# Kernel tuning notes

Measured on AMD Instinct MI355X. Metric: run time of the kernel, lower is better.

Reference implementation:

```python
import jax, jax.numpy as jnp
import numpy as np

N_IN, N_REC, T, BATCH = 128, 512, 1000, 64
ALPHA = 0.2
SIGMA = float(np.sqrt(2.0 / ALPHA) * 0.05)  # sqrt(2/alpha)*sigma_rec
EI_RATIO = 0.8
W_REC_GAIN = 1.0


def setup_inputs() -> dict:
    key = jax.random.key(0)
    k_x, k_n = jax.random.split(key)
    rng = np.random.RandomState(0)
    # w_in init: randn/sqrt(n_in)
    w_in = (rng.randn(N_IN, N_REC) / np.sqrt(N_IN)).astype(np.float32)
    # w_rec init 'randgauss' with Dale's law: abs, inhibitory rows scaled
    n_ex = int(N_REC * EI_RATIO)
    w_rec0 = W_REC_GAIN * rng.randn(N_REC, N_REC) / np.sqrt(N_REC)
    w_rec0 = np.abs(w_rec0)
    w_rec0[n_ex:, :] *= EI_RATIO / (1.0 - EI_RATIO)
    w_rec = w_rec0.astype(np.float32)
    ei_vec = np.concatenate([np.ones(n_ex), -np.ones(N_REC - n_ex)]).astype(np.float32)
    ei_mask = np.diag(ei_vec)
    autapse_mask = np.ones((N_REC, N_REC), dtype=np.float32)
    np.fill_diagonal(autapse_mask, 0.0)
    x = jax.random.normal(k_x, (BATCH, T, N_IN), dtype=jnp.float32)
    # pre-scaled noise: randn * sigma, one draw per timestep (matches torch.randn_like(h)*sigma)
    noise = jax.random.normal(k_n, (BATCH, T, N_REC), dtype=jnp.float32) * SIGMA
    return {
        "x": x,
        "w_in": jnp.asarray(w_in),
        "w_rec": jnp.asarray(w_rec),
        "b_rec": jnp.zeros((N_REC,), dtype=jnp.float32),
        "ei_mask": jnp.asarray(ei_mask),
        "autapse_mask": jnp.asarray(autapse_mask),
        "noise": noise,
    }


def reference(x, w_in, w_rec, b_rec, ei_mask, autapse_mask, noise):
    # Effective recurrent weight, computed ONCE (torch code recomputes each step)
    w_eff = ei_mask @ (w_rec * autapse_mask)          # (n_rec, n_rec)
    inp_all = jnp.einsum("bti,ir->btr", x, w_in)       # precompute input projection
    xs = (jnp.swapaxes(inp_all, 0, 1), jnp.swapaxes(noise, 0, 1))  # (T,b,r)
    h0 = jnp.zeros((x.shape[0], w_rec.shape[0]), dtype=x.dtype)

    def step(h, xt):
        inp_t, noise_t = xt
        pre = inp_t + h @ w_eff + b_rec + noise_t
        h_new = (1.0 - ALPHA) * h + ALPHA * jax.nn.relu(pre)
        return h_new, h_new

    _, h_all = jax.lax.scan(step, h0, xs)              # (T, batch, n_rec)
    return jnp.swapaxes(h_all, 0, 1)                   # (batch, T, n_rec)
```

## Files before the change

### kernel.cpp

```cpp
#include <hip/hip_runtime.h>

#define T_STEPS 1000
#define NIN     128
#define NREC    512
#define NBATCH  64
#define ALPHA   0.2f

#define NSLICE  4
#define SCOLS   128
#define NGRP    8
#define KPER    64

#define WS_W_OFF      0
#define WS_COMM_OFF   (1u << 20)
#define COMM_U64      (NBATCH * NREC)
#define COMM_BYTES    (2 * COMM_U64 * 8)
#define WS_COMM2_OFF  (WS_COMM_OFF + COMM_BYTES)
#define WS_NEEDED_LLC (WS_COMM_OFF + COMM_BYTES)
#define WS_NEEDED_DUAL (WS_COMM2_OFF + COMM_BYTES)

#define LDS_BARRIER() do {                                        \
    asm volatile("s_waitcnt lgkmcnt(0)" ::: "memory");            \
    __builtin_amdgcn_s_barrier();                                 \
    asm volatile("" ::: "memory");                                \
} while (0)

__device__ __forceinline__ unsigned long long ld_l2(
        const unsigned long long* p) {
    unsigned long long r;
    asm volatile("global_load_dwordx2 %0, %1, off sc0\n\t"
                 "s_waitcnt vmcnt(0)"
                 : "=v"(r) : "v"(p) : "memory");
    return r;
}
__device__ __forceinline__ void st_l2(unsigned long long* p,
                                      unsigned long long v) {
    asm volatile("global_store_dwordx2 %0, %1, off"
                 :: "v"(p), "v"(v) : "memory");
}
__device__ __forceinline__ unsigned long long ld_llc(
        const unsigned long long* p) {
    return __hip_atomic_load(p, __ATOMIC_RELAXED, __HIP_MEMORY_SCOPE_AGENT);
}
__device__ __forceinline__ void st_llc(unsigned long long* p,
                                       unsigned long long v) {
    __hip_atomic_store(p, v, __ATOMIC_RELAXED, __HIP_MEMORY_SCOPE_AGENT);
}

__global__ void weff_kernel(const float* __restrict__ w_rec,
                            const float* __restrict__ ei_mask,
                            const float* __restrict__ autapse,
                            float* __restrict__ w_eff) {
    int idx = blockIdx.x * blockDim.x + threadIdx.x;
    if (idx < NREC * NREC) {
        int row = idx >> 9;
        float ei = ei_mask[row * NREC + row];
        w_eff[idx] = ei * w_rec[idx] * autapse[idx];
    }
}

__global__ __launch_bounds__(1024) void gemm_in_kernel(
        const float* __restrict__ x,
        const float* __restrict__ w_in,
        const float* __restrict__ b_rec,
        float* __restrict__ io) {
    __shared__ float xs[32][NIN];

    const int tid = threadIdx.x;
    const int m0  = blockIdx.x * 32;

    {
        const float4* src = reinterpret_cast<const float4*>(x + (size_t)m0 * NIN);
        reinterpret_cast<float4*>(&xs[0][0])[tid] = src[tid];
    }
    __syncthreads();

    const int j0 = tid & 255;
    const int j1 = j0 + 256;
    const int rg = tid >> 8;

    float acc[8][2];
#pragma unroll
    for (int i = 0; i < 8; ++i) { acc[i][0] = 0.f; acc[i][1] = 0.f; }

#pragma unroll 4
    for (int k = 0; k < NIN; ++k) {
        float wv0 = w_in[k * NREC + j0];
        float wv1 = w_in[k * NREC + j1];
#pragma unroll
        for (int i = 0; i < 8; ++i) {
            float xv = xs[rg * 8 + i][k];
            acc[i][0] = fmaf(xv, wv0, acc[i][0]);
            acc[i][1] = fmaf(xv, wv1, acc[i][1]);
        }
    }

    const float br0 = b_rec[j0];
    const float br1 = b_rec[j1];
#pragma unroll
    for (int i = 0; i < 8; ++i) {
        size_t ro = (size_t)(m0 + rg * 8 + i) * NREC;
        io[ro + j0] = acc[i][0] + br0;
        io[ro + j1] = acc[i][1] + br1;
    }
}

__global__ __launch_bounds__(1024, 4) void rnn_coop(
        const float* __restrict__ W,
        const float* __restrict__ noise,
        float* __restrict__ io,
        unsigned long long* __restrict__ comm,
        unsigned long long* __restrict__ comm2) {
    __shared__ __align__(16) float h_lds[NREC];
    __shared__ float part[NGRP * SCOLS];

    const int tid = threadIdx.x;
    const int bid = blockIdx.x;
    const int b   = (bid & 7) + 8 * (bid >> 5);
    const int s   = (bid >> 3) & 3;
    const int jl  = tid & (SCOLS - 1);
    const int g   = tid >> 7;
    const int ln  = tid & 63;
    const int jg  = s * SCOLS + jl;
    const bool remote = (g >> 1) != s;
    const int cslot = g * KPER + ln;
    const bool use_l2 = (comm2 != nullptr);

    float Wr[KPER];
    {
        const float* wp = W + (size_t)(g * KPER) * NREC + jg;
#pragma unroll
        for (int u = 0; u < KPER; ++u)
            Wr[u] = wp[(size_t)u * NREC];
    }
#pragma unroll
    for (int u = 0; u < KPER; ++u)
        asm volatile("" : "+v"(Wr[u]));

    if (tid < NREC) h_lds[tid] = 0.f;
    __syncthreads();

    float hj = 0.f;
    const size_t iobase = (size_t)b * T_STEPS * NREC + jg;
    const unsigned long long* cbase  = comm  + (size_t)b * NREC + cslot;
    const unsigned long long* cbase2 = comm2 + (size_t)b * NREC + cslot;
    unsigned long long* cwr  = comm  + (size_t)b * NREC + jg;
    unsigned long long* cwr2 = comm2 + (size_t)b * NREC + jg;

    float inp = 0.f, nz = 0.f;
    if (tid < SCOLS) { inp = io[iobase]; nz = noise[iobase]; }

    for (int t = 0; t < T_STEPS; ++t) {
        const size_t off = iobase + (size_t)t * NREC;

        float inp_n = 0.f, nz_n = 0.f;
        if (t + 1 < T_STEPS && tid < SCOLS) {
            inp_n = io[off + NREC];
            nz_n  = noise[off + NREC];
        }

        if (t > 0 && remote) {
            const size_t po = (size_t)(t & 1) * COMM_U64;
            unsigned long long v;
            if (use_l2) {
                v = ld_l2(cbase2 + po);
                while ((int)(unsigned)(v >> 32) < t) {
                    v = ld_llc(cbase + po);
                    if ((int)(unsigned)(v >> 32) >= t) break;
                    v = ld_l2(cbase2 + po);
                }
            } else {
                v = ld_llc(cbase + po);
                while ((int)(unsigned)(v >> 32) < t)
                    v = ld_llc(cbase + po);
            }
            asm volatile("" ::: "memory");
            h_lds[cslot] = __uint_as_float((unsigned)(v & 0xffffffffu));
        }

        float a0 = 0.f, a1 = 0.f, a2 = 0.f, a3 = 0.f;
        const float4* h4 = reinterpret_cast<const float4*>(&h_lds[g * KPER]);
#pragma unroll
        for (int u = 0; u < KPER / 4; ++u) {
            float4 hv = h4[u];
            a0 = fmaf(hv.x, Wr[4 * u + 0], a0);
            a1 = fmaf(hv.y, Wr[4 * u + 1], a1);
            a2 = fmaf(hv.z, Wr[4 * u + 2], a2);
            a3 = fmaf(hv.w, Wr[4 * u + 3], a3);
        }
        part[g * SCOLS + jl] = (a0 + a1) + (a2 + a3);
        LDS_BARRIER();

        if (tid < SCOLS) {
            float pre = inp + nz;
#pragma unroll
            for (int q = 0; q < NGRP; ++q)
                pre += part[q * SCOLS + jl];
            float hnew = (1.f - ALPHA) * hj + ALPHA * fmaxf(pre, 0.f);
            hj = hnew;
            h_lds[jg] = hnew;
            unsigned long long pv =
                ((unsigned long long)(unsigned)(t + 1) << 32) |
                (unsigned long long)__float_as_uint(hnew);
            const size_t po = (size_t)((t + 1) & 1) * COMM_U64;
            if (use_l2) st_l2(cwr2 + po, pv);
            st_llc(cwr + po, pv);
            io[off] = hnew;
        }
        inp = inp_n; nz = nz_n;
        LDS_BARRIER();
    }
}

__global__ __launch_bounds__(1024) void rnn_kernel(
        const float* __restrict__ W,
        const float* __restrict__ noise,
        float* __restrict__ io) {
    __shared__ float h[NREC];
    __shared__ float part2[NREC];

    const int tid  = threadIdx.x;
    const int j    = tid & (NREC - 1);
    const int half = tid >> 9;
    const int b    = blockIdx.x;

    if (tid < NREC) h[tid] = 0.f;
    float hj = 0.f;
    __syncthreads();

    const int kb = half * 256;
    const float* wp = W + (size_t)kb * NREC + j;
    const size_t base = (size_t)b * T_STEPS * NREC + j;

    for (int t = 0; t < T_STEPS; ++t) {
        const size_t off = base + (size_t)t * NREC;
        float acc = (half == 0) ? (io[off] + noise[off]) : 0.f;
#pragma unroll
        for (int ku = 0; ku < 256; ku += 16) {
            float w[16];
#pragma unroll
            for (int u = 0; u < 16; ++u) w[u] = wp[(size_t)(ku + u) * NREC];
#pragma unroll
            for (int u = 0; u < 16; ++u) acc = fmaf(h[kb + ku + u], w[u], acc);
        }
        if (half == 1) part2[j] = acc;
        __syncthreads();
        if (half == 0) {
            float pre  = acc + part2[j];
            float hnew = (1.f - ALPHA) * hj + ALPHA * fmaxf(pre, 0.f);
            io[off] = hnew;
            h[j] = hnew;
            hj = hnew;
        }
        __syncthreads();
    }
}

extern "C" void kernel_launch(void* const* d_in, const int* in_sizes, int n_in,
                              void* d_out, int out_size, void* d_ws, size_t ws_size,
                              hipStream_t stream) {
    const float* x       = (const float*)d_in[0];
    const float* w_in    = (const float*)d_in[1];
    const float* w_rec   = (const float*)d_in[2];
    const float* b_rec   = (const float*)d_in[3];
    const float* ei_mask = (const float*)d_in[4];
    const float* autapse = (const float*)d_in[5];
    const float* noise   = (const float*)d_in[6];
    float* out = (float*)d_out;

    char* ws = (char*)d_ws;
    float* W = (float*)(ws + WS_W_OFF);
    unsigned long long* comm  = (unsigned long long*)(ws + WS_COMM_OFF);
    unsigned long long* comm2 = (unsigned long long*)(ws + WS_COMM2_OFF);

    weff_kernel<<<dim3((NREC * NREC + 255) / 256), dim3(256), 0, stream>>>(
        w_rec, ei_mask, autapse, W);

    gemm_in_kernel<<<dim3(64000 / 32), dim3(1024), 0, stream>>>(
        x, w_in, b_rec, out);

    if (ws_size >= (size_t)WS_NEEDED_DUAL) {
        hipMemsetAsync(comm, 0, 2 * COMM_BYTES, stream);
        void* args[] = {(void*)&W, (void*)&noise, (void*)&out,
                        (void*)&comm, (void*)&comm2};
        hipLaunchCooperativeKernel(reinterpret_cast<void*>(rnn_coop),
                                   dim3(NBATCH * NSLICE), dim3(1024),
                                   args, 0, stream);
    } else if (ws_size >= (size_t)WS_NEEDED_LLC) {
        hipMemsetAsync(comm, 0, COMM_BYTES, stream);
        unsigned long long* nul = nullptr;
        void* args[] = {(void*)&W, (void*)&noise, (void*)&out,
                        (void*)&comm, (void*)&nul};
        hipLaunchCooperativeKernel(reinterpret_cast<void*>(rnn_coop),
                                   dim3(NBATCH * NSLICE), dim3(1024),
                                   args, 0, stream);
    } else {
        rnn_kernel<<<dim3(NBATCH), dim3(1024), 0, stream>>>(W, noise, out);
    }
}
```

Baseline: 1.754 ms.

## Offload next-step input/noise prefetch to non-remote waves via LDS double buffer

Moves the per-step prefetch of the next timestep's input projection and noise from the 128 finalizing threads to the 256 local (non-remote) threads, staged through a double-buffered LDS array. The finalizing wave no longer carries global-load latency on the critical path. It also changes the spin-wait polling to hit the L2 copy three times for every LLC probe. The risk is extra LDS traffic, and polling the LLC less often could delay noticing a new value when the L2 copy is stale.

```diff
diff --git a/kernel.cpp b/kernel.cpp
--- a/kernel.cpp
+++ b/kernel.cpp
@@ -113,6 +113,7 @@
         unsigned long long* __restrict__ comm2) {
     __shared__ __align__(16) float h_lds[NREC];
     __shared__ float part[NGRP * SCOLS];
+    __shared__ float ldsin[2][2][SCOLS];
 
     const int tid = threadIdx.x;
     const int bid = blockIdx.x;
@@ -126,6 +127,13 @@
     const int cslot = g * KPER + ln;
     const bool use_l2 = (comm2 != nullptr);
 
+    const int  lt        = tid - s * 256;
+    const bool is_loader = (lt >= 0) && (lt < 256);
+    const int  lwhich    = (lt >> 7) & 1;
+    const int  lcol      = lt & (SCOLS - 1);
+    const float* lsrc    = lwhich ? noise : io;
+    const size_t lbase   = (size_t)b * T_STEPS * NREC + s * SCOLS + lcol;
+
     float Wr[KPER];
     {
         const float* wp = W + (size_t)(g * KPER) * NREC + jg;
@@ -138,6 +146,7 @@
         asm volatile("" : "+v"(Wr[u]));
 
     if (tid < NREC) h_lds[tid] = 0.f;
+    if (is_loader) ldsin[0][lwhich][lcol] = lsrc[lbase];
     __syncthreads();
 
     float hj = 0.f;
@@ -147,27 +156,26 @@
     unsigned long long* cwr  = comm  + (size_t)b * NREC + jg;
     unsigned long long* cwr2 = comm2 + (size_t)b * NREC + jg;
 
-    float inp = 0.f, nz = 0.f;
-    if (tid < SCOLS) { inp = io[iobase]; nz = noise[iobase]; }
-
     for (int t = 0; t < T_STEPS; ++t) {
-        const size_t off = iobase + (size_t)t * NREC;
-
-        float inp_n = 0.f, nz_n = 0.f;
-        if (t + 1 < T_STEPS && tid < SCOLS) {
-            inp_n = io[off + NREC];
-            nz_n  = noise[off + NREC];
-        }
+        const int p = t & 1;
+
+        float lv = 0.f;
+        const bool lactive = is_loader && (t + 1 < T_STEPS);
+        if (lactive)
+            lv = lsrc[lbase + (size_t)(t + 1) * NREC];
 
         if (t > 0 && remote) {
-            const size_t po = (size_t)(t & 1) * COMM_U64;
+            const size_t po = (size_t)p * COMM_U64;
             unsigned long long v;
             if (use_l2) {
                 v = ld_l2(cbase2 + po);
+                int it = 0;
                 while ((int)(unsigned)(v >> 32) < t) {
-                    v = ld_llc(cbase + po);
-                    if ((int)(unsigned)(v >> 32) >= t) break;
-                    v = ld_l2(cbase2 + po);
+                    if ((++it & 3) == 0) {
+                        v = ld_llc(cbase + po);
+                    } else {
+                        v = ld_l2(cbase2 + po);
+                    }
                 }
             } else {
                 v = ld_llc(cbase + po);
@@ -192,6 +200,8 @@
         LDS_BARRIER();
 
         if (tid < SCOLS) {
+            float inp = ldsin[p][0][jl];
+            float nz  = ldsin[p][1][jl];
             float pre = inp + nz;
 #pragma unroll
             for (int q = 0; q < NGRP; ++q)
@@ -205,9 +215,12 @@
             const size_t po = (size_t)((t + 1) & 1) * COMM_U64;
             if (use_l2) st_l2(cwr2 + po, pv);
             st_llc(cwr + po, pv);
-            io[off] = hnew;
-        }
-        inp = inp_n; nz = nz_n;
+            io[iobase + (size_t)t * NREC] = hnew;
+        }
+
+        if (lactive)
+            ldsin[p ^ 1][lwhich][lcol] = lv;
+
         LDS_BARRIER();
     }
 }
```

Result: slower. 2.330 ms (+32.9%).

## Broadcast hidden state via wave readlane instead of LDS staging in coop RNN

Applied to the files above, without the earlier changes.

Each wave now loads its 64 hidden values into one register per lane, either by polling the remote comm buffer or from a small own-slice LDS array. It then broadcasts them with readlane into the FMA loop, replacing the full 512-float LDS h buffer and the float4 LDS reads. The thread-to-column mapping changes so each wave covers 64 columns of one K-group. The next step's input and noise prefetch moves to after the store, inside the leader branch. This removes LDS write/read traffic and the serial dependence on LDS before the dot product, but readlane is scalar-path work and the prefetch is no longer overlapped with the poll.

```diff
diff --git a/kernel.cpp b/kernel.cpp
--- a/kernel.cpp
+++ b/kernel.cpp
@@ -111,20 +111,22 @@
         float* __restrict__ io,
         unsigned long long* __restrict__ comm,
         unsigned long long* __restrict__ comm2) {
-    __shared__ __align__(16) float h_lds[NREC];
-    __shared__ float part[NGRP * SCOLS];
+    __shared__ float h_own[SCOLS];
+    __shared__ float part[NGRP][SCOLS];
 
     const int tid = threadIdx.x;
     const int bid = blockIdx.x;
     const int b   = (bid & 7) + 8 * (bid >> 5);
     const int s   = (bid >> 3) & 3;
-    const int jl  = tid & (SCOLS - 1);
-    const int g   = tid >> 7;
+    const int w   = tid >> 6;
     const int ln  = tid & 63;
-    const int jg  = s * SCOLS + jl;
-    const bool remote = (g >> 1) != s;
-    const int cslot = g * KPER + ln;
-    const bool use_l2 = (comm2 != nullptr);
+    const int g   = w >> 1;
+    const int c   = w & 1;
+    const int col = c * 64 + ln;
+    const int jg  = s * SCOLS + col;
+    const bool own       = (w >> 2) == s;
+    const bool is_leader = own && ((w & 2) == 0);
+    const bool use_l2    = (comm2 != nullptr);
 
     float Wr[KPER];
     {
@@ -137,77 +139,73 @@
     for (int u = 0; u < KPER; ++u)
         asm volatile("" : "+v"(Wr[u]));
 
-    if (tid < NREC) h_lds[tid] = 0.f;
-    __syncthreads();
-
     float hj = 0.f;
     const size_t iobase = (size_t)b * T_STEPS * NREC + jg;
-    const unsigned long long* cbase  = comm  + (size_t)b * NREC + cslot;
-    const unsigned long long* cbase2 = comm2 + (size_t)b * NREC + cslot;
+    const unsigned long long* cpoll  = comm  + (size_t)b * NREC + g * KPER + ln;
+    const unsigned long long* cpoll2 = comm2 + (size_t)b * NREC + g * KPER + ln;
     unsigned long long* cwr  = comm  + (size_t)b * NREC + jg;
     unsigned long long* cwr2 = comm2 + (size_t)b * NREC + jg;
 
     float inp = 0.f, nz = 0.f;
-    if (tid < SCOLS) { inp = io[iobase]; nz = noise[iobase]; }
+    if (is_leader) { inp = io[iobase]; nz = noise[iobase]; }
 
     for (int t = 0; t < T_STEPS; ++t) {
-        const size_t off = iobase + (size_t)t * NREC;
-
-        float inp_n = 0.f, nz_n = 0.f;
-        if (t + 1 < T_STEPS && tid < SCOLS) {
-            inp_n = io[off + NREC];
-            nz_n  = noise[off + NREC];
-        }
-
-        if (t > 0 && remote) {
+        float hval;
+        if (t == 0) {
+            hval = 0.f;
+        } else if (own) {
+            hval = h_own[(g & 1) * KPER + ln];
+        } else {
             const size_t po = (size_t)(t & 1) * COMM_U64;
             unsigned long long v;
             if (use_l2) {
-                v = ld_l2(cbase2 + po);
+                v = ld_l2(cpoll2 + po);
                 while ((int)(unsigned)(v >> 32) < t) {
-                    v = ld_llc(cbase + po);
+                    v = ld_llc(cpoll + po);
                     if ((int)(unsigned)(v >> 32) >= t) break;
-                    v = ld_l2(cbase2 + po);
+                    v = ld_l2(cpoll2 + po);
                 }
             } else {
-                v = ld_llc(cbase + po);
+                v = ld_llc(cpoll + po);
                 while ((int)(unsigned)(v >> 32) < t)
-                    v = ld_llc(cbase + po);
+                    v = ld_llc(cpoll + po);
             }
-            asm volatile("" ::: "memory");
-            h_lds[cslot] = __uint_as_float((unsigned)(v & 0xffffffffu));
-        }
-
-        float a0 = 0.f, a1 = 0.f, a2 = 0.f, a3 = 0.f;
-        const float4* h4 = reinterpret_cast<const float4*>(&h_lds[g * KPER]);
-#pragma unroll
-        for (int u = 0; u < KPER / 4; ++u) {
-            float4 hv = h4[u];
-            a0 = fmaf(hv.x, Wr[4 * u + 0], a0);
-            a1 = fmaf(hv.y, Wr[4 * u + 1], a1);
-            a2 = fmaf(hv.z, Wr[4 * u + 2], a2);
-            a3 = fmaf(hv.w, Wr[4 * u + 3], a3);
-        }
-        part[g * SCOLS + jl] = (a0 + a1) + (a2 + a3);
+            hval = __uint_as_float((unsigned)(v & 0xffffffffu));
+        }
+
+        float a0 = 0.f, a1 = 0.f;
+#pragma unroll
+        for (int u = 0; u < KPER; u += 2) {
+            float h0 = __uint_as_float(
+                __builtin_amdgcn_readlane(__float_as_uint(hval), u));
+            float h1 = __uint_as_float(
+                __builtin_amdgcn_readlane(__float_as_uint(hval), u + 1));
+            a0 = fmaf(h0, Wr[u],     a0);
+            a1 = fmaf(h1, Wr[u + 1], a1);
+        }
+        part[g][col] = a0 + a1;
         LDS_BARRIER();
 
-        if (tid < SCOLS) {
+        if (is_leader) {
             float pre = inp + nz;
 #pragma unroll
             for (int q = 0; q < NGRP; ++q)
-                pre += part[q * SCOLS + jl];
+                pre += part[q][col];
             float hnew = (1.f - ALPHA) * hj + ALPHA * fmaxf(pre, 0.f);
             hj = hnew;
-            h_lds[jg] = hnew;
+            h_own[col] = hnew;
             unsigned long long pv =
                 ((unsigned long long)(unsigned)(t + 1) << 32) |
                 (unsigned long long)__float_as_uint(hnew);
             const size_t po = (size_t)((t + 1) & 1) * COMM_U64;
             if (use_l2) st_l2(cwr2 + po, pv);
             st_llc(cwr + po, pv);
-            io[off] = hnew;
-        }
-        inp = inp_n; nz = nz_n;
+            io[iobase + (size_t)t * NREC] = hnew;
+            if (t + 1 < T_STEPS) {
+                inp = io[iobase + (size_t)(t + 1) * NREC];
+                nz  = noise[iobase + (size_t)(t + 1) * NREC];
+            }
+        }
         LDS_BARRIER();
     }
 }
@@ -237,11 +235,11 @@
         float acc = (half == 0) ? (io[off] + noise[off]) : 0.f;
 #pragma unroll
         for (int ku = 0; ku < 256; ku += 16) {
-            float w[16];
-#pragma unroll
-            for (int u = 0; u < 16; ++u) w[u] = wp[(size_t)(ku + u) * NREC];
-#pragma unroll
-            for (int u = 0; u < 16; ++u) acc = fmaf(h[kb + ku + u], w[u], acc);
+            float wv[16];
+#pragma unroll
+            for (int u = 0; u < 16; ++u) wv[u] = wp[(size_t)(ku + u) * NREC];
+#pragma unroll
+            for (int u = 0; u < 16; ++u) acc = fmaf(h[kb + ku + u], wv[u], acc);
         }
         if (half == 1) part2[j] = acc;
         __syncthreads();
```

After: 1.676 ms. 4.4% less time.
